# Performance work log

Measured on AMD Instinct MI355X. Metric: run time of the kernel, lower is better.

## Reference

```python
import jax, jax.numpy as jnp
import numpy as np

DEPTH, C, HS, NH, WS, B = 10, 128, 512, 8, 2, 4096


def _sincos_1d(embed_dim, pos):
    omega = np.arange(embed_dim // 2, dtype=np.float64)
    omega /= embed_dim / 2.0
    omega = 1.0 / 10000 ** omega
    out = np.einsum('m,d->md', pos.reshape(-1), omega)
    return np.concatenate([np.sin(out), np.cos(out)], axis=1)


def _sincos_pos_embed(embed_dim, grid_size):
    g = np.arange(grid_size, dtype=np.float32)
    grid = np.stack(np.meshgrid(g, g), axis=0).reshape(2, -1)
    emb_h = _sincos_1d(embed_dim // 2, grid[0])
    emb_w = _sincos_1d(embed_dim // 2, grid[1])
    return np.concatenate([emb_h, emb_w], axis=1)  # (16, HS)


def _encode_board(x):
    # x: (B,128) int piece ids -> (B,12,8,8) one-hot planes (vectorized encodeBoard)
    x = x.reshape(-1, 2, 8, 8)
    pieces = jnp.arange(1, 7)
    white = (x[:, 0, None, :, :] == pieces[None, :, None, None]).astype(jnp.float32)
    black = (x[:, 1, None, :, :] == pieces[None, :, None, None]).astype(jnp.float32)
    return jnp.concatenate([white, black], axis=1)


def _conv3x3(x, w, b):
    y = jax.lax.conv_general_dilated(x, w, (1, 1), 'SAME',
                                     dimension_numbers=('NCHW', 'OIHW', 'NCHW'))
    return y + b[None, :, None, None]


def _bn(x, g, b, eps=1e-5):
    # training-mode BatchNorm2d: per-batch stats over (N,H,W)
    m = x.mean((0, 2, 3), keepdims=True)
    v = x.var((0, 2, 3), keepdims=True)
    return (x - m) * jax.lax.rsqrt(v + eps) * g[None, :, None, None] + b[None, :, None, None]


def _ln(x, eps=1e-6):
    m = x.mean(-1, keepdims=True)
    v = x.var(-1, keepdims=True)
    return (x - m) * jax.lax.rsqrt(v + eps)


def _window_partition(x, ws):
    b, c, h, w = x.shape
    x = x.reshape(b, c, h // ws, ws, w // ws, ws)
    x = x.transpose(0, 2, 4, 3, 5, 1)  # b h w p1 p2 c
    return x.reshape(b, (h // ws) * (w // ws), ws * ws * c)


def _window_reverse(win, ws, h, w):
    b, n, d = win.shape
    c = d // (ws * ws)
    x = win.reshape(b, h // ws, w // ws, ws, ws, c)
    x = x.transpose(0, 5, 1, 3, 2, 4)  # b c h p1 w p2
    return x.reshape(b, c, h, w)


def _attention(t, qkv_w, qkv_b, proj_w, proj_b):
    b, n, d = t.shape
    hd = d // NH
    qkv = (t @ qkv_w + qkv_b).reshape(b, n, 3, NH, hd)
    q, k, v = jnp.moveaxis(qkv, 2, 0)  # each (b,n,NH,hd)
    attn = jax.nn.softmax(jnp.einsum('bqhd,bkhd->bhqk', q * hd ** -0.5, k), axis=-1)
    out = jnp.einsum('bhqk,bkhd->bqhd', attn, v).reshape(b, n, d)
    return out @ proj_w + proj_b


def _block(x, pos, p):
    (rb1_w, rb1_b, g1, b1, rb2_w, rb2_b, g2, b2,
     qkv_w, qkv_b, proj_w, proj_b, f1_w, f1_b, f2_w, f2_b) = p
    h, w = x.shape[2], x.shape[3]
    z = _bn(_conv3x3(jax.nn.relu(x), rb1_w, rb1_b), g1, b1)
    z = _bn(_conv3x3(jax.nn.relu(z), rb2_w, rb2_b), g2, b2)
    x = x + z
    t = _window_partition(x, WS) + pos
    t = t + _ln(_attention(t, qkv_w, qkv_b, proj_w, proj_b))
    t = t + _ln(jax.nn.relu(t @ f1_w + f1_b) @ f2_w + f2_b)
    return _window_reverse(t, WS, h, w)


def _forward(x, pos_embed, conv1_w, conv1_b, blk, lin1_w, lin1_b, lin2_w, lin2_b):
    h = _conv3x3(_encode_board(x), conv1_w, conv1_b)

    def step(h, p):
        return _block(h, pos_embed, p), None

    h, _ = jax.lax.scan(step, h, blk)
    feat = h.transpose(0, 2, 3, 1).reshape(h.shape[0], -1)  # B (H W C)
    logits = jax.nn.relu(feat @ lin1_w + lin1_b) @ lin2_w + lin2_b
    return jax.nn.softmax(logits, axis=1)


def setup_inputs() -> dict:
    key = jax.random.key(0)
    ks = jax.random.split(key, 16)
    n = lambda k, shp: jax.random.normal(k, shp, dtype=jnp.float32) * 0.02
    inp = {}
    inp['x'] = jax.random.randint(ks[0], (B, 128), 0, 7)
    inp['pos_embed'] = jnp.asarray(_sincos_pos_embed(HS, 8 // WS), dtype=jnp.float32)[None]
    inp['conv1_w'] = n(ks[1], (C, 12, 3, 3))
    inp['conv1_b'] = jnp.zeros((C,), jnp.float32)
    inp['rb1_w'] = n(ks[2], (DEPTH, C, C, 3, 3)); inp['rb1_b'] = jnp.zeros((DEPTH, C), jnp.float32)
    inp['bn1_g'] = jnp.ones((DEPTH, C), jnp.float32); inp['bn1_b'] = jnp.zeros((DEPTH, C), jnp.float32)
    inp['rb2_w'] = n(ks[3], (DEPTH, C, C, 3, 3)); inp['rb2_b'] = jnp.zeros((DEPTH, C), jnp.float32)
    inp['bn2_g'] = jnp.ones((DEPTH, C), jnp.float32); inp['bn2_b'] = jnp.zeros((DEPTH, C), jnp.float32)
    inp['qkv_w'] = n(ks[4], (DEPTH, HS, 3 * HS)); inp['qkv_b'] = jnp.zeros((DEPTH, 3 * HS), jnp.float32)
    inp['proj_w'] = n(ks[5], (DEPTH, HS, HS)); inp['proj_b'] = jnp.zeros((DEPTH, HS), jnp.float32)
    inp['fc1_w'] = n(ks[6], (DEPTH, HS, HS)); inp['fc1_b'] = jnp.zeros((DEPTH, HS), jnp.float32)
    inp['fc2_w'] = n(ks[7], (DEPTH, HS, HS)); inp['fc2_b'] = jnp.zeros((DEPTH, HS), jnp.float32)
    inp['lin1_w'] = n(ks[8], (C * 64, 1024)); inp['lin1_b'] = jnp.zeros((1024,), jnp.float32)
    inp['lin2_w'] = n(ks[9], (1024, 640)); inp['lin2_b'] = jnp.zeros((640,), jnp.float32)
    return inp


def reference(x, pos_embed, conv1_w, conv1_b, rb1_w, rb1_b, bn1_g, bn1_b,
              rb2_w, rb2_b, bn2_g, bn2_b, qkv_w, qkv_b, proj_w, proj_b,
              fc1_w, fc1_b, fc2_w, fc2_b, lin1_w, lin1_b, lin2_w, lin2_b):
    blk = (rb1_w, rb1_b, bn1_g, bn1_b, rb2_w, rb2_b, bn2_g, bn2_b,
           qkv_w, qkv_b, proj_w, proj_b, fc1_w, fc1_b, fc2_w, fc2_b)
    return _forward(x, pos_embed, conv1_w, conv1_b, blk, lin1_w, lin1_b, lin2_w, lin2_b)
```

## Files before the change

### kernel.cpp

```cpp
#include <hip/hip_runtime.h>
#include <hip/hip_fp16.h>
#include <math.h>


#define NBATCH 4096
#define NPOSR  (NBATCH*64)
#define CH     1024
#define CHT    (CH*16)

#define OFF_ACT   0
#define OFF_BIG2  33554432
#define OFF_WT1   (OFF_BIG2 + 16777216)
#define OFF_WTA   (OFF_WT1 + 13824)
#define OFF_WTB   (OFF_WTA + 737280)
#define OFF_WTT   (OFF_WTB + 737280)
#define OFF_STATS (OFF_WTT + 786432)
#define OFF_BNP   (OFF_STATS + 256)
#define OFF_BIAS  (OFF_BNP + 256)
#define WS_NEED_FLOATS (OFF_BIAS + 1536)

#define H_QKVB 0
#define H_ATT  25165824
#define H_PRJ  0
#define H_T2H  8388608
#define H_LOG  8388608

#define T_QKV  0
#define T_PRJ  786432
#define T_F1   1048576
#define T_F2   1310720

typedef _Float16 f16x8 __attribute__((ext_vector_type(8)));
typedef _Float16 f16x4 __attribute__((ext_vector_type(4)));
typedef float f32x4 __attribute__((ext_vector_type(4)));

__device__ inline f32x4 vzero4() { f32x4 z; z[0]=0.f; z[1]=0.f; z[2]=0.f; z[3]=0.f; return z; }

__device__ inline float4 ld_half4(const __half* p) {
  float2 a = __half22float2(*(const __half2*)p);
  float2 b = __half22float2(*(const __half2*)(p + 2));
  return make_float4(a.x, a.y, b.x, b.y);
}

__global__ void k_zero(float* __restrict__ s) { s[threadIdx.x] = 0.f; }

__global__ void k_sentinel(float* __restrict__ out, int n, float val) {
  for (int i = blockIdx.x*blockDim.x + threadIdx.x; i < n; i += gridDim.x*blockDim.x)
    out[i] = val;
}

__global__ void k_wprep(const float* __restrict__ src, float* __restrict__ dst, int L, int Cin) {
  int total = L * 128 * Cin * 9;
  for (int idx = blockIdx.x*blockDim.x + threadIdx.x; idx < total; idx += gridDim.x*blockDim.x) {
    int kk = idx % 9; int t2 = idx / 9;
    int ci = t2 % Cin; t2 /= Cin;
    int co = t2 % 128; int l  = t2 / 128;
    dst[((size_t)(l*9 + kk)*Cin + ci)*128 + co] = src[idx];
  }
}

__global__ void k_wprep16(const float* __restrict__ src, __half* __restrict__ dst, int L) {
  int total = L * 128 * 128 * 9;
  for (int idx = blockIdx.x*blockDim.x + threadIdx.x; idx < total; idx += gridDim.x*blockDim.x) {
    int kk = idx % 9; int t2 = idx / 9;
    int ci = t2 % 128; t2 /= 128;
    int co = t2 % 128; int l  = t2 / 128;
    dst[((size_t)(l*128 + co))*1152 + kk*128 + ci] = __float2half(src[idx]);
  }
}

__global__ void k_wt16(const float* __restrict__ W, __half* __restrict__ WT, int K, int N) {
  int total = K * N;
  for (int idx = blockIdx.x*blockDim.x + threadIdx.x; idx < total; idx += gridDim.x*blockDim.x) {
    int k = idx / N, n = idx % N;
    WT[(size_t)n*K + k] = __float2half(W[idx]);
  }
}

__global__ void k_wt16x4(const float* __restrict__ Wq, const float* __restrict__ Wp,
                         const float* __restrict__ W1, const float* __restrict__ W2,
                         const float* __restrict__ bq,
                         __half* __restrict__ wTt, float* __restrict__ biasbuf) {
  int gid0 = blockIdx.x*blockDim.x + threadIdx.x;
  if (gid0 < 1536) biasbuf[gid0] = bq[gid0] * (gid0 < 512 ? 0.125f : 1.f);
  const int TOT = 786432 + 3*262144;
  for (int idx = gid0; idx < TOT; idx += gridDim.x*blockDim.x) {
    if (idx < 786432) {
      int k = idx / 1536, n = idx % 1536;
      float v = Wq[idx] * (n < 512 ? 0.125f : 1.f);
      wTt[T_QKV + (size_t)n*512 + k] = __float2half(v);
    } else {
      int r0 = idx - 786432;
      int s = r0 / 262144, r = r0 % 262144;
      int k = r / 512, n = r % 512;
      const float* W = (s == 0) ? Wp : (s == 1) ? W1 : W2;
      wTt[T_PRJ + s*262144 + (size_t)n*512 + k] = __float2half(W[r]);
    }
  }
}

__global__ __launch_bounds__(256) void k_conv1(const int* __restrict__ xin,
    const float* __restrict__ wT1, const float* __restrict__ b1,
    float* __restrict__ out) {
  __shared__ int s_w[64], s_b[64];
  int b = blockIdx.x, t = threadIdx.x;
  if (t < 64) { s_w[t] = xin[b*128 + t]; s_b[t] = xin[b*128 + 64 + t]; }
  __syncthreads();
  int p = t >> 2, i = t & 3;
  int y = p >> 3, x = p & 7;
  float acc[32];
  #pragma unroll
  for (int j = 0; j < 32; ++j) acc[j] = b1[i*32 + j];
  #pragma unroll
  for (int kk = 0; kk < 9; ++kk) {
    int ny = y + kk/3 - 1, nx = x + kk%3 - 1;
    if (ny < 0 || ny > 7 || nx < 0 || nx > 7) continue;
    int np = ny*8 + nx;
    int wp = s_w[np], bp = s_b[np];
    if (wp >= 1 && wp <= 6) {
      const float* w = &wT1[(size_t)(kk*12 + (wp-1))*128 + i*32];
      #pragma unroll
      for (int j = 0; j < 32; ++j) acc[j] += w[j];
    }
    if (bp >= 1 && bp <= 6) {
      const float* w = &wT1[(size_t)(kk*12 + 6 + (bp-1))*128 + i*32];
      #pragma unroll
      for (int j = 0; j < 32; ++j) acc[j] += w[j];
    }
  }
  float* o = &out[((size_t)b*64 + p)*128 + i*32];
  #pragma unroll
  for (int j = 0; j < 8; ++j)
    *(float4*)&o[j*4] = make_float4(acc[j*4], acc[j*4+1], acc[j*4+2], acc[j*4+3]);
}

__device__ inline float cvt_in(float v) { return v; }
__device__ inline float cvt_in(__half v) { return __half2float(v); }

#define IMG_W 136

template<typename TIN>
__global__ __launch_bounds__(256) void k_conv_mfma(const TIN* __restrict__ in,
    const __half* __restrict__ wT , const float* __restrict__ bias,
    const float* __restrict__ bnp, int use_bn, __half* __restrict__ out,
    float* __restrict__ stats) {
  __shared__ __align__(16) _Float16 s_img[2*65*IMG_W];
  __shared__ __align__(16) _Float16 s_B[128][68];
  __shared__ float s_sum[128], s_sq[128];
  int b2 = blockIdx.x, t = threadIdx.x;
  for (int idx4 = t; idx4 < 4096; idx4 += 256) {
    int img = idx4 >> 11, rr = (idx4 >> 5) & 63, c4 = (idx4 & 31) * 4;
    const TIN* src = &in[((size_t)(b2*2 + img)*64 + rr)*128 + c4];
    float v0 = cvt_in(src[0]), v1 = cvt_in(src[1]), v2 = cvt_in(src[2]), v3 = cvt_in(src[3]);
    if (use_bn) {
      v0 = bnp[c4+0]*v0 + bnp[128+c4+0];
      v1 = bnp[c4+1]*v1 + bnp[128+c4+1];
      v2 = bnp[c4+2]*v2 + bnp[128+c4+2];
      v3 = bnp[c4+3]*v3 + bnp[128+c4+3];
    }
    f16x4 h;
    h[0] = (_Float16)fmaxf(v0, 0.f); h[1] = (_Float16)fmaxf(v1, 0.f);
    h[2] = (_Float16)fmaxf(v2, 0.f); h[3] = (_Float16)fmaxf(v3, 0.f);
    *(f16x4*)&s_img[(img*65 + rr)*IMG_W + c4] = h;
  }
  {
    int img = t >> 7, c = t & 127;
    s_img[(img*65 + 64)*IMG_W + c] = (_Float16)0.f;
    if (t < 128) { s_sum[t] = 0.f; s_sq[t] = 0.f; }
  }
  int w = t >> 6, lane = t & 63;
  int wm = (w >> 1)*64, wn = (w & 1)*64;
  int fr = lane & 15, fq = lane >> 4;
  int imgo[4], yy[4], xx_[4];
  #pragma unroll
  for (int mt = 0; mt < 4; ++mt) {
    int r = wm + mt*16 + fr;
    imgo[mt] = r >> 6; int p = r & 63; yy[mt] = p >> 3; xx_[mt] = p & 7;
  }
  f32x4 acc[4][4];
  #pragma unroll
  for (int mt = 0; mt < 4; ++mt)
    #pragma unroll
    for (int nt = 0; nt < 4; ++nt) acc[mt][nt] = vzero4();
  int sn = t >> 1, skh2 = (t & 1) * 32;
  const __half* wrow = &wT[(size_t)sn*1152];
  for (int kk = 0; kk < 9; ++kk) {
    int dy = kk/3 - 1, dx = kk%3 - 1;
    const _Float16* abase[4];
    #pragma unroll
    for (int mt = 0; mt < 4; ++mt) {
      int ny = yy[mt] + dy, nx = xx_[mt] + dx;
      int row = ((unsigned)ny < 8u && (unsigned)nx < 8u) ? (ny*8 + nx) : 64;
      abase[mt] = &s_img[(imgo[mt]*65 + row)*IMG_W];
    }
    #pragma unroll
    for (int half = 0; half < 2; ++half) {
      int kb = kk*128 + half*64 + skh2;
      __syncthreads();
      *(ulonglong2*)&s_B[sn][skh2+0]  = *(const ulonglong2*)&wrow[kb + 0];
      *(ulonglong2*)&s_B[sn][skh2+8]  = *(const ulonglong2*)&wrow[kb + 8];
      *(ulonglong2*)&s_B[sn][skh2+16] = *(const ulonglong2*)&wrow[kb + 16];
      *(ulonglong2*)&s_B[sn][skh2+24] = *(const ulonglong2*)&wrow[kb + 24];
      __syncthreads();
      #pragma unroll
      for (int ks2 = 0; ks2 < 2; ++ks2) {
        f16x8 af[4], bf[4];
        #pragma unroll
        for (int mt = 0; mt < 4; ++mt) af[mt] = *(const f16x8*)&abase[mt][half*64 + ks2*32 + fq*8];
        #pragma unroll
        for (int nt = 0; nt < 4; ++nt) bf[nt] = *(const f16x8*)&s_B[wn + nt*16 + fr][ks2*32 + fq*8];
        #pragma unroll
        for (int mt = 0; mt < 4; ++mt)
          #pragma unroll
          for (int nt = 0; nt < 4; ++nt)
            acc[mt][nt] = __builtin_amdgcn_mfma_f32_16x16x32_f16(af[mt], bf[nt], acc[mt][nt], 0, 0, 0);
      }
    }
  }
  #pragma unroll
  for (int nt = 0; nt < 4; ++nt) {
    int col = wn + nt*16 + fr;
    float bv = bias[col];
    float s = 0.f, q = 0.f;
    #pragma unroll
    for (int mt = 0; mt < 4; ++mt) {
      int rbase = wm + mt*16 + fq*4;
      #pragma unroll
      for (int j = 0; j < 4; ++j) {
        int r = rbase + j;
        int img = r >> 6, p = r & 63;
        float v = acc[mt][nt][j] + bv;
        s += v; q += v*v;
        out[((size_t)(b2*2 + img)*64 + p)*128 + col] = __float2half(v);
      }
    }
    s += __shfl_xor(s, 16); s += __shfl_xor(s, 32);
    q += __shfl_xor(q, 16); q += __shfl_xor(q, 32);
    if (fq == 0) { atomicAdd(&s_sum[col], s); atomicAdd(&s_sq[col], q); }
  }
  __syncthreads();
  if (t < 128) {
    atomicAdd(&stats[t], s_sum[t]);
    atomicAdd(&stats[128 + t], s_sq[t]);
  }
}

__global__ void k_bnfin(float* __restrict__ stats, const float* __restrict__ g,
                        const float* __restrict__ bb, float* __restrict__ bnp) {
  int c = threadIdx.x;
  const float invN = 1.f / (float)NPOSR;
  float m = stats[c] * invN;
  float v = stats[128+c] * invN - m*m;
  float sc = g[c] * rsqrtf(v + 1e-5f);
  bnp[c] = sc;
  bnp[128+c] = bb[c] - m*sc;
  stats[c] = 0.f; stats[128+c] = 0.f;
}

__global__ __launch_bounds__(256) void k_make_t(float* __restrict__ act,
    const __half* __restrict__ z1h, const float* __restrict__ bnp,
    const float* __restrict__ pos) {
  __shared__ float s_t[8192];
  int b = blockIdx.x, t = threadIdx.x;
  for (int idx4 = t; idx4 < 2048; idx4 += 256) {
    int n = idx4 >> 7, d4 = idx4 & 127;
    int d = d4*4, c = d & 127, q = d >> 7;
    int y = ((n>>2)<<1) + (q>>1), xx = ((n&3)<<1) + (q&1);
    size_t sp = ((size_t)b*64 + y*8 + xx)*128 + c;
    float4 a  = *(const float4*)&act[sp];
    float4 z  = ld_half4(&z1h[sp]);
    float4 sc = *(const float4*)&bnp[c];
    float4 sh = *(const float4*)&bnp[128+c];
    float4 pe = *(const float4*)&pos[n*512 + d];
    float4 o;
    o.x = a.x + sc.x*z.x + sh.x + pe.x;
    o.y = a.y + sc.y*z.y + sh.y + pe.y;
    o.z = a.z + sc.z*z.z + sh.z + pe.z;
    o.w = a.w + sc.w*z.w + sh.w + pe.w;
    *(float4*)&s_t[n*512 + d] = o;
  }
  __syncthreads();
  for (int idx4 = t; idx4 < 2048; idx4 += 256)
    *(float4*)&act[(size_t)b*8192 + idx4*4] = *(float4*)&s_t[idx4*4];
}

#define QS 1544

__global__ __launch_bounds__(256) void k_attn16(const __half* __restrict__ qkvbuf,
    __half* __restrict__ attnout) {
  __shared__ __align__(16) _Float16 s_qkv[16][QS];
  __shared__ float S[8][16][17];
  int img = blockIdx.x, t = threadIdx.x;
  const __half* src = qkvbuf + (size_t)img*16*1536;
  #pragma unroll
  for (int i = 0; i < 12; ++i) {
    int lin = t + i*256;
    int row = lin / 192, c8 = lin % 192;
    *(f16x8*)&s_qkv[row][c8*8] = *(const f16x8*)&src[(size_t)row*1536 + c8*8];
  }
  __syncthreads();
  {
    int h = t >> 5, qi = (t >> 1) & 15, ko = (t & 1) * 8;
    int rot = t & 31;
    float acc[8];
    #pragma unroll
    for (int k = 0; k < 8; ++k) acc[k] = 0.f;
    const __half2* qr = (const __half2*)&s_qkv[qi][h*64];
    for (int i2 = 0; i2 < 32; ++i2) {
      int d2 = (i2 + rot) & 31;
      float2 q2 = __half22float2(qr[d2]);
      #pragma unroll
      for (int k = 0; k < 8; ++k) {
        float2 k2 = __half22float2(*(const __half2*)&s_qkv[ko + k][512 + h*64 + d2*2]);
        acc[k] += q2.x*k2.x + q2.y*k2.y;
      }
    }
    #pragma unroll
    for (int k = 0; k < 8; ++k) S[h][qi][ko + k] = acc[k];
  }
  __syncthreads();
  if (t < 128) {
    int h = t >> 4, qi = t & 15;
    float* Sr = S[h][qi];
    float mx = -1e30f;
    #pragma unroll
    for (int ki = 0; ki < 16; ++ki) mx = fmaxf(mx, Sr[ki]);
    float sm = 0.f; float e[16];
    #pragma unroll
    for (int ki = 0; ki < 16; ++ki) { e[ki] = expf(Sr[ki] - mx); sm += e[ki]; }
    float inv = 1.f / sm;
    #pragma unroll
    for (int ki = 0; ki < 16; ++ki) Sr[ki] = e[ki]*inv;
  }
  __syncthreads();
  {
    int qi = t >> 4, rem = t & 15;
    int h = rem >> 1, dhb = (rem & 1) * 32;
    int rot = (t >> 2) & 15;
    float P[16];
    #pragma unroll
    for (int k = 0; k < 16; ++k) P[k] = S[h][qi][(k + rot) & 15];
    __half* orow = attnout + ((size_t)img*16 + qi)*512 + h*64 + dhb;
    #pragma unroll
    for (int j = 0; j < 16; ++j) {
      int dh = dhb + 2*j;
      float a0 = 0.f, a1 = 0.f;
      #pragma unroll
      for (int kk2 = 0; kk2 < 16; ++kk2) {
        int ki = (kk2 + rot) & 15;
        float2 v2 = __half22float2(*(const __half2*)&s_qkv[ki][1024 + h*64 + dh]);
        a0 += P[kk2]*v2.x; a1 += P[kk2]*v2.y;
      }
      *(__half2*)&orow[2*j] = __floats2half2_rn(a0, a1);
    }
  }
}

template<int A16, int B16, int RELU, int OUT16>
__global__ __launch_bounds__(256) void k_mgemm(const void* __restrict__ Ap,
    const void* __restrict__ Bp, const float* __restrict__ bias,
    void* __restrict__ Cp, int M, int N, int K) {
  __shared__ _Float16 sA[128][40];
  __shared__ _Float16 sB[128][40];
  int t = threadIdx.x;
  int bm = blockIdx.x * 128, bn = blockIdx.y * 128;
  int w = t >> 6, lane = t & 63;
  int wm = (w >> 1) * 64, wn = (w & 1) * 64;
  int fr = lane & 15, fq = lane >> 4;
  f32x4 acc[4][4];
  #pragma unroll
  for (int mt = 0; mt < 4; ++mt)
    #pragma unroll
    for (int nt = 0; nt < 4; ++nt) acc[mt][nt] = vzero4();
  int srow = t >> 1, skh = (t & 1) * 16;
  for (int k0 = 0; k0 < K; k0 += 32) {
    if (A16) {
      const __half* A = (const __half*)Ap;
      const ulonglong2* src = (const ulonglong2*)&A[(size_t)(bm + srow)*K + k0 + skh];
      *(ulonglong2*)&sA[srow][skh]   = src[0];
      *(ulonglong2*)&sA[srow][skh+8] = src[1];
    } else {
      const float* A = (const float*)Ap;
      const float4* src = (const float4*)&A[(size_t)(bm + srow)*K + k0 + skh];
      float4 v0 = src[0], v1 = src[1], v2 = src[2], v3 = src[3];
      f16x8 h0, h1;
      h0[0]=(_Float16)v0.x; h0[1]=(_Float16)v0.y; h0[2]=(_Float16)v0.z; h0[3]=(_Float16)v0.w;
      h0[4]=(_Float16)v1.x; h0[5]=(_Float16)v1.y; h0[6]=(_Float16)v1.z; h0[7]=(_Float16)v1.w;
      h1[0]=(_Float16)v2.x; h1[1]=(_Float16)v2.y; h1[2]=(_Float16)v2.z; h1[3]=(_Float16)v2.w;
      h1[4]=(_Float16)v3.x; h1[5]=(_Float16)v3.y; h1[6]=(_Float16)v3.z; h1[7]=(_Float16)v3.w;
      *(f16x8*)&sA[srow][skh]   = h0;
      *(f16x8*)&sA[srow][skh+8] = h1;
    }
    if (B16) {
      const __half* BT = (const __half*)Bp;
      const ulonglong2* src = (const ulonglong2*)&BT[(size_t)(bn + srow)*K + k0 + skh];
      *(ulonglong2*)&sB[srow][skh]   = src[0];
      *(ulonglong2*)&sB[srow][skh+8] = src[1];
    } else {
      const float* B = (const float*)Bp;
      int kr = t >> 3, n0 = (t & 7) * 16;
      #pragma unroll
      for (int g = 0; g < 4; ++g) {
        float4 v = *(const float4*)&B[(size_t)(k0 + kr)*N + bn + n0 + g*4];
        sB[n0+g*4+0][kr] = (_Float16)v.x;
        sB[n0+g*4+1][kr] = (_Float16)v.y;
        sB[n0+g*4+2][kr] = (_Float16)v.z;
        sB[n0+g*4+3][kr] = (_Float16)v.w;
      }
    }
    __syncthreads();
    f16x8 af[4], bf[4];
    #pragma unroll
    for (int mt = 0; mt < 4; ++mt) af[mt] = *(const f16x8*)&sA[wm + mt*16 + fr][fq*8];
    #pragma unroll
    for (int nt = 0; nt < 4; ++nt) bf[nt] = *(const f16x8*)&sB[wn + nt*16 + fr][fq*8];
    #pragma unroll
    for (int mt = 0; mt < 4; ++mt)
      #pragma unroll
      for (int nt = 0; nt < 4; ++nt)
        acc[mt][nt] = __builtin_amdgcn_mfma_f32_16x16x32_f16(af[mt], bf[nt], acc[mt][nt], 0, 0, 0);
    __syncthreads();
  }
  #pragma unroll
  for (int mt = 0; mt < 4; ++mt)
    #pragma unroll
    for (int nt = 0; nt < 4; ++nt) {
      int col = bn + wn + nt*16 + fr;
      float bv = bias[col];
      #pragma unroll
      for (int j = 0; j < 4; ++j) {
        int row = bm + wm + mt*16 + fq*4 + j;
        float v = acc[mt][nt][j] + bv;
        if (RELU) v = fmaxf(v, 0.f);
        if (OUT16) ((__half*)Cp)[(size_t)row*N + col] = __float2half(v);
        else       ((float*)Cp)[(size_t)row*N + col] = v;
      }
    }
}

__global__ __launch_bounds__(256) void k_lnres(const __half* __restrict__ pout,
    float* __restrict__ tact, __half* __restrict__ t2h) {
  int t = threadIdx.x;
  int tok = blockIdx.x*4 + (t >> 6);
  int lane = t & 63;
  f16x8 hv = *(const f16x8*)&pout[(size_t)tok*512 + lane*8];
  float v[8]; float s1 = 0.f, s2 = 0.f;
  #pragma unroll
  for (int j = 0; j < 8; ++j) { v[j] = (float)hv[j]; s1 += v[j]; s2 += v[j]*v[j]; }
  #pragma unroll
  for (int m = 32; m >= 1; m >>= 1) { s1 += __shfl_xor(s1, m); s2 += __shfl_xor(s2, m); }
  float mean = s1 * (1.f/512.f);
  float var  = s2 * (1.f/512.f) - mean*mean;
  float rs = rsqrtf(var + 1e-6f);
  float* ar = &tact[(size_t)tok*512 + lane*8];
  f16x8 o16;
  #pragma unroll
  for (int j = 0; j < 8; ++j) {
    float t2 = ar[j] + (v[j] - mean)*rs;
    ar[j] = t2;
    o16[j] = (_Float16)t2;
  }
  *(f16x8*)&t2h[(size_t)tok*512 + lane*8] = o16;
}

__global__ __launch_bounds__(256) void k_lnres2(const __half* __restrict__ fout,
    float* __restrict__ actimg) {
  __shared__ float s_t2[8192];
  int bimg = blockIdx.x, t = threadIdx.x;
  int lane = t & 63;
  for (int tg = 0; tg < 4; ++tg) {
    int n = tg*4 + (t >> 6);
    size_t row = (size_t)bimg*16 + n;
    f16x8 hv = *(const f16x8*)&fout[row*512 + lane*8];
    float v[8]; float s1 = 0.f, s2 = 0.f;
    #pragma unroll
    for (int j = 0; j < 8; ++j) { v[j] = (float)hv[j]; s1 += v[j]; s2 += v[j]*v[j]; }
    #pragma unroll
    for (int m = 32; m >= 1; m >>= 1) { s1 += __shfl_xor(s1, m); s2 += __shfl_xor(s2, m); }
    float mean = s1 * (1.f/512.f);
    float var  = s2 * (1.f/512.f) - mean*mean;
    float rs = rsqrtf(var + 1e-6f);
    const float* ar = &actimg[row*512 + lane*8];
    #pragma unroll
    for (int j = 0; j < 8; ++j) s_t2[n*512 + lane*8 + j] = ar[j] + (v[j] - mean)*rs;
  }
  __syncthreads();
  for (int idx = t; idx < 2048; idx += 256) {
    int p = idx >> 5, c = (idx & 31)*4;
    int y = p >> 3, x = p & 7;
    int n = (y >> 1)*4 + (x >> 1);
    int d = ((y & 1)*2 + (x & 1))*128 + c;
    *(float4*)&actimg[(size_t)bimg*8192 + p*128 + c] = *(float4*)&s_t2[n*512 + d];
  }
}

__global__ __launch_bounds__(256) void k_softmax(const float* __restrict__ logits, float* __restrict__ out) {
  int b = blockIdx.x, t = threadIdx.x;
  __shared__ float red[256];
  float m = -1e30f;
  for (int j = t; j < 640; j += 256) m = fmaxf(m, logits[(size_t)b*640 + j]);
  red[t] = m; __syncthreads();
  for (int s = 128; s > 0; s >>= 1) { if (t < s) red[t] = fmaxf(red[t], red[t+s]); __syncthreads(); }
  m = red[0]; __syncthreads();
  float sum = 0.f;
  for (int j = t; j < 640; j += 256) sum += expf(logits[(size_t)b*640 + j] - m);
  red[t] = sum; __syncthreads();
  for (int s = 128; s > 0; s >>= 1) { if (t < s) red[t] += red[t+s]; __syncthreads(); }
  float inv = 1.f / red[0];
  for (int j = t; j < 640; j += 256) out[(size_t)b*640 + j] = expf(logits[(size_t)b*640 + j] - m) * inv;
}

extern "C" void kernel_launch(void* const* d_in, const int* in_sizes, int n_in,
                              void* d_out, int out_size, void* d_ws, size_t ws_size,
                              hipStream_t stream) {
  (void)in_sizes; (void)n_in;
  float* out = (float*)d_out;
  if (ws_size < (size_t)WS_NEED_FLOATS * 4) {
    k_sentinel<<<2048, 256, 0, stream>>>(out, out_size, (float)(ws_size >> 20));
    return;
  }

  const int*   x       = (const int*)d_in[0];
  const float* pos     = (const float*)d_in[1];
  const float* conv1_w = (const float*)d_in[2];
  const float* conv1_b = (const float*)d_in[3];
  const float* rb1_w   = (const float*)d_in[4];
  const float* rb1_b   = (const float*)d_in[5];
  const float* bn1_g   = (const float*)d_in[6];
  const float* bn1_b   = (const float*)d_in[7];
  const float* rb2_w   = (const float*)d_in[8];
  const float* rb2_b   = (const float*)d_in[9];
  const float* bn2_g   = (const float*)d_in[10];
  const float* bn2_b   = (const float*)d_in[11];
  const float* qkv_w   = (const float*)d_in[12];
  const float* qkv_b   = (const float*)d_in[13];
  const float* proj_w  = (const float*)d_in[14];
  const float* proj_b  = (const float*)d_in[15];
  const float* fc1_w   = (const float*)d_in[16];
  const float* fc1_b   = (const float*)d_in[17];
  const float* fc2_w   = (const float*)d_in[18];
  const float* fc2_b   = (const float*)d_in[19];
  const float* lin1_w  = (const float*)d_in[20];
  const float* lin1_b  = (const float*)d_in[21];
  const float* lin2_w  = (const float*)d_in[22];
  const float* lin2_b  = (const float*)d_in[23];

  float*  ws    = (float*)d_ws;
  float*  act   = ws + OFF_ACT;
  __half* big2h = (__half*)(ws + OFF_BIG2);
  float*  wT1   = ws + OFF_WT1;
  __half* wTa16 = (__half*)(ws + OFF_WTA);
  __half* wTb16 = (__half*)(ws + OFF_WTB);
  __half* wTt   = (__half*)(ws + OFF_WTT);
  float*  stats = ws + OFF_STATS;
  float*  bnp   = ws + OFF_BNP;
  float*  biasbuf = ws + OFF_BIAS;

  __half* z1h     = big2h;
  __half* qkvbuf  = big2h + H_QKVB;
  __half* attnout = big2h + H_ATT;
  __half* projout = big2h + H_PRJ;
  __half* t2h     = big2h + H_T2H;
  __half* h1      = attnout;
  __half* fc2out  = projout;
  __half* qkvT    = wTt + T_QKV;
  __half* projT   = wTt + T_PRJ;
  __half* fc1T    = wTt + T_F1;
  __half* fc2T    = wTt + T_F2;
  __half* L1h     = big2h;
  float*  logits  = (float*)(big2h + H_LOG);
  __half* lin2T   = wTt;

  k_zero<<<1, 256, 0, stream>>>(stats);
  k_wprep<<<64, 256, 0, stream>>>(conv1_w, wT1, 1, 12);
  k_wprep16<<<2048, 256, 0, stream>>>(rb1_w, wTa16, 10);
  k_wprep16<<<2048, 256, 0, stream>>>(rb2_w, wTb16, 10);
  k_conv1<<<NBATCH, 256, 0, stream>>>(x, wT1, conv1_b, act);

  for (int l = 0; l < 10; ++l) {
    k_conv_mfma<float><<<NBATCH/2, 256, 0, stream>>>(act, wTa16 + (size_t)l*147456,
        rb1_b + l*128, (const float*)nullptr, 0, z1h, stats);
    k_bnfin<<<1, 128, 0, stream>>>(stats, bn1_g + l*128, bn1_b + l*128, bnp);
    k_conv_mfma<__half><<<NBATCH/2, 256, 0, stream>>>(z1h, wTb16 + (size_t)l*147456,
        rb2_b + l*128, bnp, 1, z1h, stats);
    k_bnfin<<<1, 128, 0, stream>>>(stats, bn2_g + l*128, bn2_b + l*128, bnp);
    k_make_t<<<NBATCH, 256, 0, stream>>>(act, z1h, bnp, pos);

    k_wt16x4<<<2048, 256, 0, stream>>>(qkv_w + (size_t)l*786432,
        proj_w + (size_t)l*262144, fc1_w + (size_t)l*262144, fc2_w + (size_t)l*262144,
        qkv_b + l*1536, wTt, biasbuf);

    for (int ch = 0; ch < NBATCH/CH; ++ch) {
      float* tchunk = act + (size_t)ch*CH*8192;
      k_mgemm<0,1,0,1><<<dim3(CHT/128, 12), 256, 0, stream>>>(tchunk, qkvT,
          biasbuf, qkvbuf, CHT, 1536, 512);
      k_attn16<<<CH, 256, 0, stream>>>(qkvbuf, attnout);
      k_mgemm<1,1,0,1><<<dim3(CHT/128, 4), 256, 0, stream>>>(attnout, projT,
          proj_b + l*512, projout, CHT, 512, 512);
      k_lnres<<<CHT/4, 256, 0, stream>>>(projout, tchunk, t2h);
      k_mgemm<1,1,1,1><<<dim3(CHT/128, 4), 256, 0, stream>>>(t2h, fc1T,
          fc1_b + l*512, h1, CHT, 512, 512);
      k_mgemm<1,1,0,1><<<dim3(CHT/128, 4), 256, 0, stream>>>(h1, fc2T,
          fc2_b + l*512, fc2out, CHT, 512, 512);
      k_lnres2<<<CH, 256, 0, stream>>>(fc2out, tchunk);
    }
  }
  k_mgemm<0,0,1,1><<<dim3(4096/128, 8), 256, 0, stream>>>(act, lin1_w, lin1_b, L1h,
      4096, 1024, 8192);
  k_wt16<<<512, 256, 0, stream>>>(lin2_w, lin2T, 1024, 640);
  k_mgemm<1,1,0,0><<<dim3(4096/128, 5), 256, 0, stream>>>(L1h, lin2T, lin2_b, logits,
      4096, 640, 1024);
  k_softmax<<<NBATCH, 256, 0, stream>>>(logits, out);
}
```

Baseline: 10.44 ms.

## Double-buffer conv and GEMM operand tiles using async global-to-LDS loads

```diff
diff --git a/kernel.cpp b/kernel.cpp
--- a/kernel.cpp
+++ b/kernel.cpp
@@ -40,6 +40,13 @@
   float2 a = __half22float2(*(const __half2*)p);
   float2 b = __half22float2(*(const __half2*)(p + 2));
   return make_float4(a.x, a.y, b.x, b.y);
+}
+
+__device__ __forceinline__ void gll16(const void* g, void* lds) {
+  __builtin_amdgcn_global_load_lds(
+      (__attribute__((address_space(1))) void*)g,
+      (__attribute__((address_space(3))) void*)lds,
+      16, 0, 0);
 }
 
 __global__ void k_zero(float* __restrict__ s) { s[threadIdx.x] = 0.f; }
@@ -145,9 +152,21 @@
     const float* __restrict__ bnp, int use_bn, __half* __restrict__ out,
     float* __restrict__ stats) {
   __shared__ __align__(16) _Float16 s_img[2*65*IMG_W];
-  __shared__ __align__(16) _Float16 s_B[128][68];
+  __shared__ __align__(16) _Float16 s_B[2][4096];
   __shared__ float s_sum[128], s_sq[128];
   int b2 = blockIdx.x, t = threadIdx.x;
+  int w = t >> 6, lane = t & 63;
+
+  auto issueB = [&](int win, int buf) {
+    #pragma unroll
+    for (int i = 0; i < 2; ++i) {
+      int rbase = (w*2 + i)*16;
+      const __half* g = &wT[(size_t)(rbase + (lane>>2))*1152 + win*32 + (lane&3)*8];
+      gll16(g, &s_B[buf][rbase*32]);
+    }
+  };
+  issueB(0, 0);
+
   for (int idx4 = t; idx4 < 4096; idx4 += 256) {
     int img = idx4 >> 11, rr = (idx4 >> 5) & 63, c4 = (idx4 & 31) * 4;
     const TIN* src = &in[((size_t)(b2*2 + img)*64 + rr)*128 + c4];
@@ -168,7 +187,6 @@
     s_img[(img*65 + 64)*IMG_W + c] = (_Float16)0.f;
     if (t < 128) { s_sum[t] = 0.f; s_sq[t] = 0.f; }
   }
-  int w = t >> 6, lane = t & 63;
   int wm = (w >> 1)*64, wn = (w & 1)*64;
   int fr = lane & 15, fq = lane >> 4;
   int imgo[4], yy[4], xx_[4];
@@ -182,8 +200,9 @@
   for (int mt = 0; mt < 4; ++mt)
     #pragma unroll
     for (int nt = 0; nt < 4; ++nt) acc[mt][nt] = vzero4();
-  int sn = t >> 1, skh2 = (t & 1) * 32;
-  const __half* wrow = &wT[(size_t)sn*1152];
+  __syncthreads();
+
+  #pragma unroll
   for (int kk = 0; kk < 9; ++kk) {
     int dy = kk/3 - 1, dx = kk%3 - 1;
     const _Float16* abase[4];
@@ -194,27 +213,21 @@
       abase[mt] = &s_img[(imgo[mt]*65 + row)*IMG_W];
     }
     #pragma unroll
-    for (int half = 0; half < 2; ++half) {
-      int kb = kk*128 + half*64 + skh2;
+    for (int q = 0; q < 4; ++q) {
+      int win = kk*4 + q;
+      int buf = win & 1;
+      if (win + 1 < 36) issueB(win + 1, buf ^ 1);
+      f16x8 af[4], bf[4];
+      #pragma unroll
+      for (int mt = 0; mt < 4; ++mt) af[mt] = *(const f16x8*)&abase[mt][q*32 + fq*8];
+      #pragma unroll
+      for (int nt = 0; nt < 4; ++nt) bf[nt] = *(const f16x8*)&s_B[buf][(wn + nt*16 + fr)*32 + fq*8];
+      #pragma unroll
+      for (int mt = 0; mt < 4; ++mt)
+        #pragma unroll
+        for (int nt = 0; nt < 4; ++nt)
+          acc[mt][nt] = __builtin_amdgcn_mfma_f32_16x16x32_f16(af[mt], bf[nt], acc[mt][nt], 0, 0, 0);
       __syncthreads();
-      *(ulonglong2*)&s_B[sn][skh2+0]  = *(const ulonglong2*)&wrow[kb + 0];
-      *(ulonglong2*)&s_B[sn][skh2+8]  = *(const ulonglong2*)&wrow[kb + 8];
-      *(ulonglong2*)&s_B[sn][skh2+16] = *(const ulonglong2*)&wrow[kb + 16];
-      *(ulonglong2*)&s_B[sn][skh2+24] = *(const ulonglong2*)&wrow[kb + 24];
-      __syncthreads();
-      #pragma unroll
-      for (int ks2 = 0; ks2 < 2; ++ks2) {
-        f16x8 af[4], bf[4];
-        #pragma unroll
-        for (int mt = 0; mt < 4; ++mt) af[mt] = *(const f16x8*)&abase[mt][half*64 + ks2*32 + fq*8];
-        #pragma unroll
-        for (int nt = 0; nt < 4; ++nt) bf[nt] = *(const f16x8*)&s_B[wn + nt*16 + fr][ks2*32 + fq*8];
-        #pragma unroll
-        for (int mt = 0; mt < 4; ++mt)
-          #pragma unroll
-          for (int nt = 0; nt < 4; ++nt)
-            acc[mt][nt] = __builtin_amdgcn_mfma_f32_16x16x32_f16(af[mt], bf[nt], acc[mt][nt], 0, 0, 0);
-      }
     }
   }
   #pragma unroll
@@ -356,73 +369,102 @@
   }
 }
 
-template<int A16, int B16, int RELU, int OUT16>
+template<int MTI, int A16, int B16, int RELU, int OUT16>
 __global__ __launch_bounds__(256) void k_mgemm(const void* __restrict__ Ap,
     const void* __restrict__ Bp, const float* __restrict__ bias,
     void* __restrict__ Cp, int M, int N, int K) {
-  __shared__ _Float16 sA[128][40];
-  __shared__ _Float16 sB[128][40];
+  constexpr int BM = MTI*32;
+  __shared__ __align__(16) _Float16 sA[2][BM*32];
+  __shared__ __align__(16) _Float16 sB[2][128*32];
   int t = threadIdx.x;
-  int bm = blockIdx.x * 128, bn = blockIdx.y * 128;
+  int bm = blockIdx.x * BM, bn = blockIdx.y * 128;
   int w = t >> 6, lane = t & 63;
-  int wm = (w >> 1) * 64, wn = (w & 1) * 64;
+  int wm = (w >> 1) * (MTI*16), wn = (w & 1) * 64;
   int fr = lane & 15, fq = lane >> 4;
-  f32x4 acc[4][4];
-  #pragma unroll
-  for (int mt = 0; mt < 4; ++mt)
-    #pragma unroll
-    for (int nt = 0; nt < 4; ++nt) acc[mt][nt] = vzero4();
-  int srow = t >> 1, skh = (t & 1) * 16;
-  for (int k0 = 0; k0 < K; k0 += 32) {
+
+  auto stageA = [&](int k0, int buf) {
     if (A16) {
       const __half* A = (const __half*)Ap;
-      const ulonglong2* src = (const ulonglong2*)&A[(size_t)(bm + srow)*K + k0 + skh];
-      *(ulonglong2*)&sA[srow][skh]   = src[0];
-      *(ulonglong2*)&sA[srow][skh+8] = src[1];
+      constexpr int NI = MTI/2;
+      #pragma unroll
+      for (int i = 0; i < NI; ++i) {
+        int rbase = (w*NI + i)*16;
+        gll16(&A[(size_t)(bm + rbase + (lane>>2))*K + k0 + (lane&3)*8],
+              &sA[buf][rbase*32]);
+      }
     } else {
       const float* A = (const float*)Ap;
-      const float4* src = (const float4*)&A[(size_t)(bm + srow)*K + k0 + skh];
-      float4 v0 = src[0], v1 = src[1], v2 = src[2], v3 = src[3];
-      f16x8 h0, h1;
-      h0[0]=(_Float16)v0.x; h0[1]=(_Float16)v0.y; h0[2]=(_Float16)v0.z; h0[3]=(_Float16)v0.w;
-      h0[4]=(_Float16)v1.x; h0[5]=(_Float16)v1.y; h0[6]=(_Float16)v1.z; h0[7]=(_Float16)v1.w;
-      h1[0]=(_Float16)v2.x; h1[1]=(_Float16)v2.y; h1[2]=(_Float16)v2.z; h1[3]=(_Float16)v2.w;
-      h1[4]=(_Float16)v3.x; h1[5]=(_Float16)v3.y; h1[6]=(_Float16)v3.z; h1[7]=(_Float16)v3.w;
-      *(f16x8*)&sA[srow][skh]   = h0;
-      *(f16x8*)&sA[srow][skh+8] = h1;
-    }
+      if (MTI == 4) {
+        int srow = t >> 1, skh = (t & 1) * 16;
+        const float4* src = (const float4*)&A[(size_t)(bm + srow)*K + k0 + skh];
+        float4 v0 = src[0], v1 = src[1], v2 = src[2], v3 = src[3];
+        f16x8 h0, h1;
+        h0[0]=(_Float16)v0.x; h0[1]=(_Float16)v0.y; h0[2]=(_Float16)v0.z; h0[3]=(_Float16)v0.w;
+        h0[4]=(_Float16)v1.x; h0[5]=(_Float16)v1.y; h0[6]=(_Float16)v1.z; h0[7]=(_Float16)v1.w;
+        h1[0]=(_Float16)v2.x; h1[1]=(_Float16)v2.y; h1[2]=(_Float16)v2.z; h1[3]=(_Float16)v2.w;
+        h1[4]=(_Float16)v3.x; h1[5]=(_Float16)v3.y; h1[6]=(_Float16)v3.z; h1[7]=(_Float16)v3.w;
+        *(f16x8*)&sA[buf][srow*32 + skh]     = h0;
+        *(f16x8*)&sA[buf][srow*32 + skh + 8] = h1;
+      } else {
+        int srow = t >> 2, g8 = (t & 3) * 8;
+        const float4* src = (const float4*)&A[(size_t)(bm + srow)*K + k0 + g8];
+        float4 v0 = src[0], v1 = src[1];
+        f16x8 h0;
+        h0[0]=(_Float16)v0.x; h0[1]=(_Float16)v0.y; h0[2]=(_Float16)v0.z; h0[3]=(_Float16)v0.w;
+        h0[4]=(_Float16)v1.x; h0[5]=(_Float16)v1.y; h0[6]=(_Float16)v1.z; h0[7]=(_Float16)v1.w;
+        *(f16x8*)&sA[buf][srow*32 + g8] = h0;
+      }
+    }
+  };
+  auto stageB = [&](int k0, int buf) {
     if (B16) {
       const __half* BT = (const __half*)Bp;
-      const ulonglong2* src = (const ulonglong2*)&BT[(size_t)(bn + srow)*K + k0 + skh];
-      *(ulonglong2*)&sB[srow][skh]   = src[0];
-      *(ulonglong2*)&sB[srow][skh+8] = src[1];
+      #pragma unroll
+      for (int i = 0; i < 2; ++i) {
+        int rbase = (w*2 + i)*16;
+        gll16(&BT[(size_t)(bn + rbase + (lane>>2))*K + k0 + (lane&3)*8],
+              &sB[buf][rbase*32]);
+      }
     } else {
       const float* B = (const float*)Bp;
       int kr = t >> 3, n0 = (t & 7) * 16;
       #pragma unroll
       for (int g = 0; g < 4; ++g) {
         float4 v = *(const float4*)&B[(size_t)(k0 + kr)*N + bn + n0 + g*4];
-        sB[n0+g*4+0][kr] = (_Float16)v.x;
-        sB[n0+g*4+1][kr] = (_Float16)v.y;
-        sB[n0+g*4+2][kr] = (_Float16)v.z;
-        sB[n0+g*4+3][kr] = (_Float16)v.w;
-      }
-    }
-    __syncthreads();
-    f16x8 af[4], bf[4];
-    #pragma unroll
-    for (int mt = 0; mt < 4; ++mt) af[mt] = *(const f16x8*)&sA[wm + mt*16 + fr][fq*8];
-    #pragma unroll
-    for (int nt = 0; nt < 4; ++nt) bf[nt] = *(const f16x8*)&sB[wn + nt*16 + fr][fq*8];
-    #pragma unroll
-    for (int mt = 0; mt < 4; ++mt)
+        sB[buf][(n0+g*4+0)*32 + kr] = (_Float16)v.x;
+        sB[buf][(n0+g*4+1)*32 + kr] = (_Float16)v.y;
+        sB[buf][(n0+g*4+2)*32 + kr] = (_Float16)v.z;
+        sB[buf][(n0+g*4+3)*32 + kr] = (_Float16)v.w;
+      }
+    }
+  };
+
+  f32x4 acc[MTI][4];
+  #pragma unroll
+  for (int mt = 0; mt < MTI; ++mt)
+    #pragma unroll
+    for (int nt = 0; nt < 4; ++nt) acc[mt][nt] = vzero4();
+
+  stageA(0, 0); stageB(0, 0);
+  __syncthreads();
+  int KW = K >> 5;
+  for (int kw = 0; kw < KW; ++kw) {
+    int buf = kw & 1;
+    if (kw + 1 < KW) { stageA((kw+1)*32, buf ^ 1); stageB((kw+1)*32, buf ^ 1); }
+    f16x8 af[MTI], bf[4];
+    #pragma unroll
+    for (int mt = 0; mt < MTI; ++mt) af[mt] = *(const f16x8*)&sA[buf][(wm + mt*16 + fr)*32 + fq*8];
+    #pragma unroll
+    for (int nt = 0; nt < 4; ++nt) bf[nt] = *(const f16x8*)&sB[buf][(wn + nt*16 + fr)*32 + fq*8];
+    #pragma unroll
+    for (int mt = 0; mt < MTI; ++mt)
       #pragma unroll
       for (int nt = 0; nt < 4; ++nt)
         acc[mt][nt] = __builtin_amdgcn_mfma_f32_16x16x32_f16(af[mt], bf[nt], acc[mt][nt], 0, 0, 0);
     __syncthreads();
   }
   #pragma unroll
-  for (int mt = 0; mt < 4; ++mt)
+  for (int mt = 0; mt < MTI; ++mt)
     #pragma unroll
     for (int nt = 0; nt < 4; ++nt) {
       int col = bn + wn + nt*16 + fr;
@@ -592,23 +634,23 @@
 
     for (int ch = 0; ch < NBATCH/CH; ++ch) {
       float* tchunk = act + (size_t)ch*CH*8192;
-      k_mgemm<0,1,0,1><<<dim3(CHT/128, 12), 256, 0, stream>>>(tchunk, qkvT,
+      k_mgemm<4,0,1,0,1><<<dim3(CHT/128, 12), 256, 0, stream>>>(tchunk, qkvT,
           biasbuf, qkvbuf, CHT, 1536, 512);
       k_attn16<<<CH, 256, 0, stream>>>(qkvbuf, attnout);
-      k_mgemm<1,1,0,1><<<dim3(CHT/128, 4), 256, 0, stream>>>(attnout, projT,
+      k_mgemm<4,1,1,0,1><<<dim3(CHT/128, 4), 256, 0, stream>>>(attnout, projT,
           proj_b + l*512, projout, CHT, 512, 512);
       k_lnres<<<CHT/4, 256, 0, stream>>>(projout, tchunk, t2h);
-      k_mgemm<1,1,1,1><<<dim3(CHT/128, 4), 256, 0, stream>>>(t2h, fc1T,
+      k_mgemm<4,1,1,1,1><<<dim3(CHT/128, 4), 256, 0, stream>>>(t2h, fc1T,
           fc1_b + l*512, h1, CHT, 512, 512);
-      k_mgemm<1,1,0,1><<<dim3(CHT/128, 4), 256, 0, stream>>>(h1, fc2T,
+      k_mgemm<4,1,1,0,1><<<dim3(CHT/128, 4), 256, 0, stream>>>(h1, fc2T,
           fc2_b + l*512, fc2out, CHT, 512, 512);
       k_lnres2<<<CH, 256, 0, stream>>>(fc2out, tchunk);
     }
   }
-  k_mgemm<0,0,1,1><<<dim3(4096/128, 8), 256, 0, stream>>>(act, lin1_w, lin1_b, L1h,
+  k_mgemm<2,0,0,1,1><<<dim3(4096/64, 8), 256, 0, stream>>>(act, lin1_w, lin1_b, L1h,
       4096, 1024, 8192);
   k_wt16<<<512, 256, 0, stream>>>(lin2_w, lin2T, 1024, 640);
-  k_mgemm<1,1,0,0><<<dim3(4096/128, 5), 256, 0, stream>>>(L1h, lin2T, lin2_b, logits,
+  k_mgemm<2,1,1,0,0><<<dim3(4096/64, 5), 256, 0, stream>>>(L1h, lin2T, lin2_b, logits,
       4096, 640, 1024);
   k_softmax<<<NBATCH, 256, 0, stream>>>(logits, out);
 }
```

Result: faster. 10.16 ms (-2.7%).
